# Optimization experiments

Measured on AMD Instinct MI355X. Metric: run time of the kernel, lower is better.

## Reference

```python
import jax, jax.numpy as jnp
import numpy as np

B, N, DIM = 4, 8192, 1024
H, DH, W = 16, 64, 128
INNER = H * DH


def setup_inputs() -> dict:
    key = jax.random.key(0)
    k0, k1, k2, k3 = jax.random.split(key, 4)
    s = 0.02
    return {
        "x": jax.random.normal(k0, (B, N, DIM), jnp.float32),
        "wq": jax.random.normal(k1, (DIM, INNER), jnp.float32) * s,
        "wkv": jax.random.normal(k2, (DIM, 2 * INNER), jnp.float32) * s,
        "wo": jax.random.normal(k3, (INNER, DIM), jnp.float32) * s,
        "bo": jnp.zeros((DIM,), jnp.float32),
    }


def reference(x, wq, wkv, wo, bo):
    b, n, _ = x.shape
    h, dh, w = H, DH, W
    scale = dh ** -0.5
    # projections (n is a multiple of w, so no padding path)
    q = x @ wq
    k, v = jnp.split(x @ wkv, 2, axis=-1)

    def to_windows(t):
        # b n (h d) -> (b h) n d -> (b h) n/w w d
        t = t.reshape(b, n, h, dh).transpose(0, 2, 1, 3)
        return t.reshape(b * h, n // w, w, dh)

    qw, kw, vw = map(to_windows, (q, k, v))

    def add_prev_window(t):
        # prepend a zero window, then each window sees [prev, current] -> j = 2w
        tp = jnp.pad(t, ((0, 0), (1, 0), (0, 0), (0, 0)))
        return jnp.concatenate([tp[:, :-1], tp[:, 1:]], axis=2)

    kw, vw = add_prev_window(kw), add_prev_window(vw)

    sim = jnp.einsum('bwid,bwjd->bwij', qw, kw) * scale  # (bh, n/w, w, 2w)
    i, j = w, 2 * w
    causal = jnp.triu(jnp.ones((i, j), bool), j - i + 1)  # masks j > i + w
    neg = -jnp.finfo(sim.dtype).max
    sim = jnp.where(causal, neg, sim)
    attn = jax.nn.softmax(sim, axis=-1)
    out = jnp.einsum('bwij,bwjd->bwid', attn, vw)  # (bh, n/w, w, dh)
    out = out.reshape(b, h, n, dh).transpose(0, 2, 1, 3).reshape(b, n, h * dh)
    return out @ wo + bo
```

## Files before the change

kernel.cpp:

```cpp
#include <hip/hip_runtime.h>
#include <stdint.h>

typedef unsigned short u16;
typedef __bf16 bf16x8 __attribute__((ext_vector_type(8)));
typedef float f32x4 __attribute__((ext_vector_type(4)));
typedef unsigned short u16x8 __attribute__((ext_vector_type(8)));

#define MFMA16(a, b, c) __builtin_amdgcn_mfma_f32_16x16x32_bf16((a), (b), (c), 0, 0, 0)

#define SEQ_N 8192
#define NWIN 64

__device__ __forceinline__ u16 f2bf(float f) {
  union { float f; uint32_t u; } v; v.f = f;
  return (u16)((v.u + 0x7fffu + ((v.u >> 16) & 1u)) >> 16);
}

__device__ __forceinline__ void load_lds16(const u16* g, u16* l) {
  __builtin_amdgcn_global_load_lds((const __attribute__((address_space(1))) void*)g,
                                   (__attribute__((address_space(3))) void*)l, 16, 0, 0);
}

__global__ __launch_bounds__(256) void cast_bf16_kernel(const float* __restrict__ src,
                                                        u16* __restrict__ dst, int n8) {
  int i = blockIdx.x * 256 + threadIdx.x;
  if (i >= n8) return;
  const float4* s = (const float4*)src + (size_t)i * 2;
  float4 a = s[0], b = s[1];
  u16x8 o;
  o[0] = f2bf(a.x); o[1] = f2bf(a.y); o[2] = f2bf(a.z); o[3] = f2bf(a.w);
  o[4] = f2bf(b.x); o[5] = f2bf(b.y); o[6] = f2bf(b.z); o[7] = f2bf(b.w);
  *((u16x8*)dst + i) = o;
}

__global__ __launch_bounds__(256) void transpose_cast_kernel(u16* __restrict__ dst,
                                                             const float* __restrict__ srcA,
                                                             const float* __restrict__ srcB,
                                                             int bcols) {
  __shared__ float tile[32][33];
  const int tx = threadIdx.x & 31, ty = threadIdx.x >> 5;
  const int n0 = blockIdx.x * 32, k0 = blockIdx.y * 32;
#pragma unroll
  for (int i = 0; i < 4; ++i) {
    int k = k0 + ty + i * 8;
    int n = n0 + tx;
    float v = (n < 1024) ? srcA[(size_t)k * 1024 + n]
                         : srcB[(size_t)k * bcols + (n - 1024)];
    tile[ty + i * 8][tx] = v;
  }
  __syncthreads();
#pragma unroll
  for (int i = 0; i < 4; ++i) {
    int n = n0 + ty + i * 8;
    int k = k0 + tx;
    dst[(size_t)n * 1024 + k] = f2bf(tile[tx][ty + i * 8]);
  }
}

template <int MODE>
__global__ __launch_bounds__(256, 2) void gemm_bt_kernel(
    const u16* __restrict__ A, const u16* __restrict__ Bt,
    u16* __restrict__ qo, u16* __restrict__ ko, u16* __restrict__ vo,
    float* __restrict__ out, const float* __restrict__ bias) {
  constexpr int K = 1024;
  __shared__ u16 As[128 * 32];
  __shared__ u16 Bs[128 * 32];
  const int tid = threadIdx.x;
  const int wave = tid >> 6, lane = tid & 63;
  const int quad = lane >> 4, l15 = lane & 15;
  const int bm = blockIdx.y, bn = blockIdx.x;
  const int wm = wave >> 1, wn = wave & 1;

  f32x4 acc[4][4] = {};

  const size_t aoff0 = (size_t)(bm * 128 + wave * 32 + (lane >> 2)) * K + (lane & 3) * 8;
  const size_t boff0 = (size_t)(bn * 128 + wave * 32 + (lane >> 2)) * K + (lane & 3) * 8;
  u16* as0 = &As[wave * 1024];
  u16* bs0 = &Bs[wave * 1024];

  for (int kt = 0; kt < K / 32; ++kt) {
    __syncthreads();
    const u16* ga = A + aoff0 + kt * 32;
    const u16* gb = Bt + boff0 + kt * 32;
    load_lds16(ga, as0);
    load_lds16(ga + 16 * K, as0 + 512);
    load_lds16(gb, bs0);
    load_lds16(gb + 16 * K, bs0 + 512);
    __syncthreads();

    bf16x8 af[4], bf[4];
#pragma unroll
    for (int mt = 0; mt < 4; ++mt)
      af[mt] = *(const bf16x8*)&As[(wm * 64 + mt * 16 + l15) * 32 + quad * 8];
#pragma unroll
    for (int nt = 0; nt < 4; ++nt)
      bf[nt] = *(const bf16x8*)&Bs[(wn * 64 + nt * 16 + l15) * 32 + quad * 8];
#pragma unroll
    for (int mt = 0; mt < 4; ++mt)
#pragma unroll
      for (int nt = 0; nt < 4; ++nt)
        acc[mt][nt] = MFMA16(af[mt], bf[nt], acc[mt][nt]);
  }

  const int row0 = bm * 128 + wm * 64;
  const int col0 = bn * 128 + wn * 64;
#pragma unroll
  for (int mt = 0; mt < 4; ++mt) {
#pragma unroll
    for (int nt = 0; nt < 4; ++nt) {
      const int col = col0 + nt * 16 + l15;
      if (MODE == 0) {
        u16* dst = (col < 1024) ? qo : ((col < 2048) ? ko : vo);
        const int cc = col & 1023;
#pragma unroll
        for (int r = 0; r < 4; ++r) {
          const int row = row0 + mt * 16 + quad * 4 + r;
          dst[(size_t)row * 1024 + cc] = f2bf(acc[mt][nt][r]);
        }
      } else {
        const float bv = bias[col];
#pragma unroll
        for (int r = 0; r < 4; ++r) {
          const int row = row0 + mt * 16 + quad * 4 + r;
          out[(size_t)row * 1024 + col] = acc[mt][nt][r] + bv;
        }
      }
    }
  }
}

__global__ __launch_bounds__(256, 2) void attn_kernel(const u16* __restrict__ qb,
                                                      const u16* __restrict__ kb,
                                                      const u16* __restrict__ vb,
                                                      u16* __restrict__ ob) {
  __shared__ u16 Vt[64][264];
  __shared__ u16 Ps[4 * 2048];
  const int tid = threadIdx.x;
  const int wave = tid >> 6, lane = tid & 63;
  const int quad = lane >> 4, l15 = lane & 15;
  const int blk = blockIdx.x;
  const int wi = blk & (NWIN - 1);
  const int bh = blk >> 6;
  const long tok0 = (long)(bh >> 4) * SEQ_N + (long)wi * 128;
  const int hoff = (bh & 15) * 64;
  const long qbase = tok0 * 1024 + hoff;
  const long kbase = (tok0 - 128) * 1024 + hoff;

  {
    const int t = tid;
    const bool pad = (wi == 0) && (t < 128);
#pragma unroll
    for (int d0 = 0; d0 < 64; d0 += 8) {
      u16x8 v8;
      if (pad) {
        v8 = (u16x8)0;
      } else {
        v8 = *(const u16x8*)(vb + (kbase + (long)t * 1024 + d0));
      }
#pragma unroll
      for (int j = 0; j < 8; ++j) Vt[d0 + j][t] = v8[j];
    }
  }

  bf16x8 qf[2][2];
#pragma unroll
  for (int mt = 0; mt < 2; ++mt)
#pragma unroll
    for (int kk = 0; kk < 2; ++kk)
      qf[mt][kk] = *(const bf16x8*)(qb + (qbase + (long)(wave * 32 + mt * 16 + l15) * 1024 +
                                          kk * 32 + quad * 8));

  f32x4 s[2][16] = {};
#pragma unroll
  for (int nt = 0; nt < 16; ++nt) {
    if (!((wi == 0) && (nt < 8))) {
      const long kt = kbase + (long)(nt * 16 + l15) * 1024;
      bf16x8 kf0 = *(const bf16x8*)(kb + (kt + quad * 8));
      bf16x8 kf1 = *(const bf16x8*)(kb + (kt + 32 + quad * 8));
#pragma unroll
      for (int mt = 0; mt < 2; ++mt) {
        s[mt][nt] = MFMA16(qf[mt][0], kf0, s[mt][nt]);
        s[mt][nt] = MFMA16(qf[mt][1], kf1, s[mt][nt]);
      }
    }
  }

#pragma unroll
  for (int mt = 0; mt < 2; ++mt) {
#pragma unroll
    for (int r = 0; r < 4; ++r) {
      const int row = wave * 32 + mt * 16 + quad * 4 + r;
      float m = -3.0e38f;
#pragma unroll
      for (int nt = 0; nt < 16; ++nt) {
        const int col = nt * 16 + l15;
        float x = s[mt][nt][r] * 0.125f;
        if (col > row + 128) x = -3.0e38f;
        s[mt][nt][r] = x;
        m = fmaxf(m, x);
      }
      m = fmaxf(m, __shfl_xor(m, 1));
      m = fmaxf(m, __shfl_xor(m, 2));
      m = fmaxf(m, __shfl_xor(m, 4));
      m = fmaxf(m, __shfl_xor(m, 8));
      float sum = 0.f;
#pragma unroll
      for (int nt = 0; nt < 16; ++nt) {
        float e = __expf(s[mt][nt][r] - m);
        s[mt][nt][r] = e;
        sum += e;
      }
      sum += __shfl_xor(sum, 1);
      sum += __shfl_xor(sum, 2);
      sum += __shfl_xor(sum, 4);
      sum += __shfl_xor(sum, 8);
      const float inv = 1.0f / sum;
#pragma unroll
      for (int nt = 0; nt < 16; ++nt) s[mt][nt][r] *= inv;
    }
  }

  __syncthreads();

  f32x4 o[2][4] = {};
#pragma unroll
  for (int ks = 0; ks < 8; ++ks) {
    u16* myP = &Ps[wave * 2048 + (ks & 1) * 1024];
#pragma unroll
    for (int mt = 0; mt < 2; ++mt)
#pragma unroll
      for (int half = 0; half < 2; ++half) {
        const int nt = ks * 2 + half;
#pragma unroll
        for (int r = 0; r < 4; ++r)
          myP[(mt * 16 + quad * 4 + r) * 32 + half * 16 + l15] = f2bf(s[mt][nt][r]);
      }
    bf16x8 pf[2];
    pf[0] = *(const bf16x8*)&myP[l15 * 32 + quad * 8];
    pf[1] = *(const bf16x8*)&myP[(16 + l15) * 32 + quad * 8];
#pragma unroll
    for (int ont = 0; ont < 4; ++ont) {
      bf16x8 vf = *(const bf16x8*)&Vt[ont * 16 + l15][ks * 32 + quad * 8];
      o[0][ont] = MFMA16(pf[0], vf, o[0][ont]);
      o[1][ont] = MFMA16(pf[1], vf, o[1][ont]);
    }
  }

#pragma unroll
  for (int mt = 0; mt < 2; ++mt)
#pragma unroll
    for (int ont = 0; ont < 4; ++ont)
#pragma unroll
      for (int r = 0; r < 4; ++r) {
        const int row = wave * 32 + mt * 16 + quad * 4 + r;
        const int col = ont * 16 + l15;
        ob[qbase + (long)row * 1024 + col] = f2bf(o[mt][ont][r]);
      }
}

extern "C" void kernel_launch(void* const* d_in, const int* in_sizes, int n_in,
                              void* d_out, int out_size, void* d_ws, size_t ws_size,
                              hipStream_t stream) {
  const float* x   = (const float*)d_in[0];
  const float* wq  = (const float*)d_in[1];
  const float* wkv = (const float*)d_in[2];
  const float* wo  = (const float*)d_in[3];
  const float* bo  = (const float*)d_in[4];
  float* out = (float*)d_out;

  const size_t XE = (size_t)4 * SEQ_N * 1024;
  u16* ws = (u16*)d_ws;
  u16* xb    = ws;
  u16* qbuf  = ws + XE;
  u16* kbuf  = ws + 2 * XE;
  u16* vbuf  = ws + 3 * XE;
  u16* wqkvT = ws + 4 * XE;
  u16* woT   = wqkvT + 3072 * 1024;
  u16* obuf  = xb;

  cast_bf16_kernel<<<16384, 256, 0, stream>>>(x, xb, (int)(XE / 8));
  transpose_cast_kernel<<<dim3(96, 32), 256, 0, stream>>>(wqkvT, wq, wkv, 2048);
  transpose_cast_kernel<<<dim3(32, 32), 256, 0, stream>>>(woT, wo, wo, 1024);
  gemm_bt_kernel<0><<<dim3(24, 256), 256, 0, stream>>>(xb, wqkvT, qbuf, kbuf, vbuf,
                                                       nullptr, nullptr);
  attn_kernel<<<4096, 256, 0, stream>>>(qbuf, kbuf, vbuf, obuf);
  gemm_bt_kernel<1><<<dim3(8, 256), 256, 0, stream>>>(obuf, woT, nullptr, nullptr, nullptr,
                                                      out, bo);
}
```

Baseline: 705.0 us.

## Replace projection GEMMs with 256x256 double-buffered 8-wave pipelined kernel

Replaces the 128x128 single-buffered GEMM with a 256x256-tile, 512-thread kernel that uses 128 KB of dynamic LDS as a double buffer for BK=64 stages. It prefetches two K-steps ahead with global_load_lds, XOR-swizzles the LDS layout to avoid bank conflicts, and interleaves LDS reads with MFMA quadrants under s_setprio and explicit waitcnt/barrier control. Block index remapping groups M tiles for L2 reuse. The aim is to hide global memory latency and raise MFMA utilization, at the cost of higher register and LDS pressure and fragile hand-placed synchronization.

```diff
diff --git a/kernel.cpp b/kernel.cpp
--- a/kernel.cpp
+++ b/kernel.cpp
@@ -11,12 +11,19 @@
 #define SEQ_N 8192
 #define NWIN 64
 
+#define BAR() __builtin_amdgcn_s_barrier()
+#define PRIO1() __builtin_amdgcn_s_setprio(1)
+#define PRIO0() __builtin_amdgcn_s_setprio(0)
+#define VM8() asm volatile("s_waitcnt vmcnt(8)" ::: "memory")
+#define VM0() asm volatile("s_waitcnt vmcnt(0)" ::: "memory")
+#define LGKM0() asm volatile("s_waitcnt lgkmcnt(0)" ::: "memory")
+
 __device__ __forceinline__ u16 f2bf(float f) {
   union { float f; uint32_t u; } v; v.f = f;
   return (u16)((v.u + 0x7fffu + ((v.u >> 16) & 1u)) >> 16);
 }
 
-__device__ __forceinline__ void load_lds16(const u16* g, u16* l) {
+__device__ __forceinline__ void load_lds16(const void* g, void* l) {
   __builtin_amdgcn_global_load_lds((const __attribute__((address_space(1))) void*)g,
                                    (__attribute__((address_space(3))) void*)l, 16, 0, 0);
 }
@@ -57,67 +64,114 @@
   }
 }
 
-template <int MODE>
-__global__ __launch_bounds__(256, 2) void gemm_bt_kernel(
+#define READ_A(MH)                                                                 \
+  _Pragma("unroll") for (int kk = 0; kk < 2; ++kk)                                 \
+  _Pragma("unroll") for (int m = 0; m < 4; ++m)                                    \
+    af[m][kk] = *(const bf16x8*)(Ard + bo + (((MH) * 64 + m * 16) << 7) + ax[kk]);
+
+#define READ_B(NH)                                                                 \
+  _Pragma("unroll") for (int kk = 0; kk < 2; ++kk)                                 \
+  _Pragma("unroll") for (int n = 0; n < 2; ++n)                                    \
+    bfr[n][kk] = *(const bf16x8*)(Brd + bo + (((NH) * 32 + n * 16) << 7) + ax[kk]);
+
+#define MFMA_QUAD(MH, NH)                                                          \
+  _Pragma("unroll") for (int kk = 0; kk < 2; ++kk)                                 \
+  _Pragma("unroll") for (int m = 0; m < 4; ++m)                                    \
+  _Pragma("unroll") for (int n = 0; n < 2; ++n)                                    \
+    acc[(MH) * 4 + m][(NH) * 2 + n] =                                              \
+        MFMA16(af[m][kk], bfr[n][kk], acc[(MH) * 4 + m][(NH) * 2 + n]);
+
+template <int NBN, int MODE>
+__global__ __launch_bounds__(512, 2) void gemm8_kernel(
     const u16* __restrict__ A, const u16* __restrict__ Bt,
     u16* __restrict__ qo, u16* __restrict__ ko, u16* __restrict__ vo,
     float* __restrict__ out, const float* __restrict__ bias) {
+  extern __shared__ char smem[];
   constexpr int K = 1024;
-  __shared__ u16 As[128 * 32];
-  __shared__ u16 Bs[128 * 32];
+  constexpr int NT = K / 64;
   const int tid = threadIdx.x;
   const int wave = tid >> 6, lane = tid & 63;
   const int quad = lane >> 4, l15 = lane & 15;
-  const int bm = blockIdx.y, bn = blockIdx.x;
-  const int wm = wave >> 1, wn = wave & 1;
-
-  f32x4 acc[4][4] = {};
-
-  const size_t aoff0 = (size_t)(bm * 128 + wave * 32 + (lane >> 2)) * K + (lane & 3) * 8;
-  const size_t boff0 = (size_t)(bn * 128 + wave * 32 + (lane >> 2)) * K + (lane & 3) * 8;
-  u16* as0 = &As[wave * 1024];
-  u16* bs0 = &Bs[wave * 1024];
-
-  for (int kt = 0; kt < K / 32; ++kt) {
-    __syncthreads();
-    const u16* ga = A + aoff0 + kt * 32;
-    const u16* gb = Bt + boff0 + kt * 32;
-    load_lds16(ga, as0);
-    load_lds16(ga + 16 * K, as0 + 512);
-    load_lds16(gb, bs0);
-    load_lds16(gb + 16 * K, bs0 + 512);
-    __syncthreads();
-
-    bf16x8 af[4], bf[4];
-#pragma unroll
-    for (int mt = 0; mt < 4; ++mt)
-      af[mt] = *(const bf16x8*)&As[(wm * 64 + mt * 16 + l15) * 32 + quad * 8];
-#pragma unroll
-    for (int nt = 0; nt < 4; ++nt)
-      bf[nt] = *(const bf16x8*)&Bs[(wn * 64 + nt * 16 + l15) * 32 + quad * 8];
-#pragma unroll
-    for (int mt = 0; mt < 4; ++mt)
-#pragma unroll
-      for (int nt = 0; nt < 4; ++nt)
-        acc[mt][nt] = MFMA16(af[mt], bf[nt], acc[mt][nt]);
-  }
-
-  const int row0 = bm * 128 + wm * 64;
-  const int col0 = bn * 128 + wn * 64;
-#pragma unroll
-  for (int mt = 0; mt < 4; ++mt) {
+  const int wm = wave >> 2, wn = wave & 3;
+
+  const int idx0 = blockIdx.x;
+  const int local = idx0 >> 3;
+  const int bn = local >> 4;
+  const int bm = ((idx0 & 7) << 4) + (local & 15);
+
+  char* const Ab = smem;
+  char* const Bb = smem + 65536;
+
+  const int sr = lane >> 3;
+  const int sg = ((lane & 7) ^ sr) * 8;
+  const u16* const gA = A + (size_t)(bm * 256 + wave * 32 + sr) * K + sg;
+  const u16* const gB = Bt + (size_t)(bn * 256 + wave * 32 + sr) * K + sg;
+  char* const lA = Ab + wave * 32 * 128;
+  char* const lB = Bb + wave * 32 * 128;
+
+  auto stage = [&](int buf, int kt) {
+#pragma unroll
+    for (int i = 0; i < 4; ++i)
+      load_lds16(gA + (size_t)kt * 64 + i * 8 * K, lA + buf * 32768 + i * 1024);
+#pragma unroll
+    for (int i = 0; i < 4; ++i)
+      load_lds16(gB + (size_t)kt * 64 + i * 8 * K, lB + buf * 32768 + i * 1024);
+  };
+
+  const int ax[2] = { (quad ^ (l15 & 7)) << 4, ((quad ^ (l15 & 7)) << 4) ^ 64 };
+  const char* const Ard = Ab + ((wm * 128 + l15) << 7);
+  const char* const Brd = Bb + ((wn * 64 + l15) << 7);
+
+  f32x4 acc[8][4] = {};
+  bf16x8 af[4][2], bfr[2][2];
+
+  stage(0, 0);
+  stage(1, 1);
+  VM8();
+  BAR();
+
+  for (int kt = 0; kt < NT; ++kt) {
+    const int buf = kt & 1;
+    const int bo = buf * 32768;
+    READ_A(0)
+    READ_B(0)
+    BAR(); LGKM0();
+    PRIO1(); MFMA_QUAD(0, 0) PRIO0();
+    BAR();
+    READ_B(1)
+    BAR(); LGKM0();
+    PRIO1(); MFMA_QUAD(0, 1) PRIO0();
+    BAR();
+    READ_A(1)
+    BAR(); LGKM0();
+    PRIO1(); MFMA_QUAD(1, 1) PRIO0();
+    BAR();
+    READ_B(0)
+    LGKM0();
+    BAR();
+    if (kt + 2 < NT) stage(buf, kt + 2);
+    PRIO1(); MFMA_QUAD(1, 0) PRIO0();
+    if (kt < NT - 1) {
+      if (kt + 2 < NT) { VM8(); } else { VM0(); }
+      BAR();
+    }
+  }
+
+  const int row0 = bm * 256 + wm * 128;
+#pragma unroll
+  for (int mt = 0; mt < 8; ++mt) {
 #pragma unroll
     for (int nt = 0; nt < 4; ++nt) {
-      const int col = col0 + nt * 16 + l15;
       if (MODE == 0) {
-        u16* dst = (col < 1024) ? qo : ((col < 2048) ? ko : vo);
-        const int cc = col & 1023;
+        u16* dst = (bn < 4) ? qo : ((bn < 8) ? ko : vo);
+        const int cc = ((bn & 3) << 8) + wn * 64 + nt * 16 + l15;
 #pragma unroll
         for (int r = 0; r < 4; ++r) {
           const int row = row0 + mt * 16 + quad * 4 + r;
           dst[(size_t)row * 1024 + cc] = f2bf(acc[mt][nt][r]);
         }
       } else {
+        const int col = bn * 256 + wn * 64 + nt * 16 + l15;
         const float bv = bias[col];
 #pragma unroll
         for (int r = 0; r < 4; ++r) {
@@ -278,12 +332,17 @@
   u16* woT   = wqkvT + 3072 * 1024;
   u16* obuf  = xb;
 
+  hipFuncSetAttribute(reinterpret_cast<const void*>(gemm8_kernel<12, 0>),
+                      hipFuncAttributeMaxDynamicSharedMemorySize, 131072);
+  hipFuncSetAttribute(reinterpret_cast<const void*>(gemm8_kernel<4, 1>),
+                      hipFuncAttributeMaxDynamicSharedMemorySize, 131072);
+
   cast_bf16_kernel<<<16384, 256, 0, stream>>>(x, xb, (int)(XE / 8));
   transpose_cast_kernel<<<dim3(96, 32), 256, 0, stream>>>(wqkvT, wq, wkv, 2048);
   transpose_cast_kernel<<<dim3(32, 32), 256, 0, stream>>>(woT, wo, wo, 1024);
-  gemm_bt_kernel<0><<<dim3(24, 256), 256, 0, stream>>>(xb, wqkvT, qbuf, kbuf, vbuf,
-                                                       nullptr, nullptr);
+  gemm8_kernel<12, 0><<<1536, 512, 131072, stream>>>(xb, wqkvT, qbuf, kbuf, vbuf,
+                                                     nullptr, nullptr);
   attn_kernel<<<4096, 256, 0, stream>>>(qbuf, kbuf, vbuf, obuf);
-  gemm_bt_kernel<1><<<dim3(8, 256), 256, 0, stream>>>(obuf, woT, nullptr, nullptr, nullptr,
-                                                      out, bo);
-}
+  gemm8_kernel<4, 1><<<512, 512, 131072, stream>>>(obuf, woT, nullptr, nullptr, nullptr,
+                                                   out, bo);
+}
```

Result: faster. 660.9 us (-6.3%).
